# Optimization experiments

Measured on AMD Instinct MI355X. Metric: run time of the kernel, lower is better.

The kernel has to match this reference:

```python
import jax, jax.numpy as jnp
import numpy as np

N_USER, N_ITEM, D = 100000, 50000, 64
H, S, B, L, SUPP, E, HID = 4, 500, 1024, 50, 10000, 1500000, 64

def setup_inputs() -> dict:
    key = jax.random.key(0)
    ks = jax.random.split(key, 24)
    f = lambda k, shp: (jax.random.normal(k, shp, jnp.float32) * 0.1)
    inp = {
        'x': jax.random.randint(ks[0], (B, 2), 0, 50000),
        'history': jax.random.randint(ks[1], (B, L), 0, N_ITEM),
        'history_len': jax.random.randint(ks[2], (B,), 1, L + 1),
        'sample_index': jax.random.randint(ks[3], (H, B, S), 0, SUPP),
        'supp_users': jax.random.randint(ks[4], (SUPP,), 0, N_USER),
        'edge_index': jax.random.randint(ks[5], (2, E), 0, 50000),
        'user_embedding': f(ks[6], (N_USER, D)),
        'item_embedding': f(ks[7], (N_ITEM, D)),
        'wq': f(ks[8], (H, D, D)),
        'wk': f(ks[9], (H, D, D)),
        'wv': f(ks[10], (H, D, D)),
        'w_out_w': f(ks[11], (H * D, D)),
        'gcn_user_w': f(ks[12], (D, D)), 'gcn_user_b': jnp.full((D,), 0.1, jnp.float32),
        'gcn_item_w': f(ks[13], (D, D)), 'gcn_item_b': jnp.full((D,), 0.1, jnp.float32),
        'l1_w': f(ks[14], (4 * D, 2 * HID)), 'l1_b': jnp.full((2 * HID,), 0.1, jnp.float32),
        'l2_w': f(ks[15], (2 * HID, HID)), 'l2_b': jnp.full((HID,), 0.1, jnp.float32),
        'l3_w': f(ks[16], (HID, 1)), 'l3_b': jnp.full((1,), 0.1, jnp.float32),
        'user_bias': jnp.zeros((N_USER, 1), jnp.float32),
        'item_bias': jnp.zeros((N_ITEM, 1), jnp.float32),
    }
    return inp


def _forward(x, history, history_len, sample_index, supp_users, edge_index,
             user_embedding, item_embedding, wq, wk, wv, w_out_w,
             gcn_user_w, gcn_user_b, gcn_item_w, gcn_item_b,
             l1_w, l1_b, l2_w, l2_b, l3_w, l3_b, user_bias, item_bias):
    user_id = x[:, 0]
    item_id = x[:, 1]
    # user init embedding: mean of history item embeddings (original sums unmasked, divides by len)
    user_init_emb = jnp.sum(item_embedding[history], axis=1) / history_len[:, None].astype(jnp.float32)  # [B,D]

    # multi-head RelationGAT over randomly sampled support users
    samp_emb = user_embedding[supp_users[sample_index]]            # [H,B,S,D]
    q = jnp.einsum('bd,hde->hbe', user_init_emb, wq)               # [H,B,D]
    k = jnp.einsum('hbsd,hde->hbse', samp_emb, wk)                 # [H,B,S,D]
    attn = jax.nn.softmax(jnp.einsum('hbe,hbse->hbs', q, k), axis=-1)
    ctx = jnp.einsum('hbs,hbse->hbe', attn, k)                     # [H,B,D]
    gat = jnp.einsum('hbe,hef->hbf', ctx, wv)                      # [H,B,D]
    gat = jnp.transpose(gat, (1, 0, 2)).reshape(gat.shape[1], -1)  # [B,H*D]
    user_emb = gat @ w_out_w                                       # [B,D]

    item_emb = item_embedding[item_id]

    # sparse GCN aggregation via segment_sum (eval mode: no edge dropout)
    eu, ei = edge_index[0], edge_index[1]
    ones_e = jnp.ones((eu.shape[0],), jnp.float32)
    agg_item = jax.ops.segment_sum(item_embedding[ei], eu, num_segments=N_USER)[user_id]
    agg_user = jax.ops.segment_sum(user_embedding[eu], ei, num_segments=N_ITEM)[item_id]
    deg_u = jax.ops.segment_sum(ones_e, eu, num_segments=N_USER)[user_id][:, None] + 1.0
    deg_i = jax.ops.segment_sum(ones_e, ei, num_segments=N_ITEM)[item_id][:, None] + 1.0
    gcn_item_h = agg_item / deg_u
    gcn_user_h = agg_user / deg_i
    gcn_user_out = jax.nn.relu(gcn_user_h @ gcn_user_w + gcn_user_b)
    gcn_item_out = jax.nn.relu(gcn_item_h @ gcn_item_w + gcn_item_b)

    feats = jnp.concatenate([user_emb * item_emb,
                             user_emb * gcn_item_out,
                             gcn_user_out * item_emb,
                             gcn_user_out * gcn_item_out], axis=-1)  # [B,4D]
    h1 = jnp.tanh(feats @ l1_w + l1_b)
    h2 = jnp.tanh(h1 @ l2_w + l2_b)
    score = (h2 @ l3_w + l3_b).reshape(-1)
    return score + user_bias[user_id].reshape(-1) + item_bias[item_id].reshape(-1)


def reference(x, history, history_len, sample_index, supp_users, edge_index,
              user_embedding, item_embedding, wq, wk, wv, w_out_w,
              gcn_user_w, gcn_user_b, gcn_item_w, gcn_item_b,
              l1_w, l1_b, l2_w, l2_b, l3_w, l3_b, user_bias, item_bias):
    return _forward(x, history, history_len, sample_index, supp_users, edge_index,
                    user_embedding, item_embedding, wq, wk, wv, w_out_w,
                    gcn_user_w, gcn_user_b, gcn_item_w, gcn_item_b,
                    l1_w, l1_b, l2_w, l2_b, l3_w, l3_b, user_bias, item_bias)
```

## Files before the change

### kernel.cpp

```cpp
#include <hip/hip_runtime.h>
#include <hip/hip_bf16.h>
#include <math.h>

#define N_USER 100000
#define N_ITEM 50000
#define D 64
#define H 4
#define S 500
#define B 1024
#define L 50
#define SUPP 10000
#define E_EDGES 1500000
#define HID 64
#define N_ID 50000
#define CAP 256

typedef _Float16 half2v __attribute__((ext_vector_type(2)));

#define SUPP_BLKS 625
#define UINIT_BLKS 256
#define PREP1_BLKS 32
#define PREP2_BLKS 64
#define REP_BLKS 4
#define B_UINIT (SUPP_BLKS)
#define B_PREP1 (B_UINIT + UINIT_BLKS)
#define B_PREP2 (B_PREP1 + PREP1_BLKS)
#define B_REP   (B_PREP2 + PREP2_BLKS)
#define SETUP_BLKS (B_REP + REP_BLKS)

__device__ __forceinline__ ushort f2h(float f) {
  _Float16 h = (_Float16)f;
  return __builtin_bit_cast(ushort, h);
}

__global__ void k_setup(const int* x, const int* history, const int* history_len,
                        const int* supp_users, const float* user_embedding,
                        const float* item_embedding, const float* wq, const float* wk,
                        const float* wv, const float* w_out_w,
                        ushort* supp_h, float* uinit, float* Mmat, float* Pmat,
                        int* user_rep, int* item_rep, int* uctr, int* ictr) {
  __shared__ float smem[64 * 65];
  int blk = blockIdx.x, tid = threadIdx.x;
  if (blk < B_UINIT) {
    int i = blk * 256 + tid;
    if (i < SUPP * 16) {
      int r = i >> 4, c = i & 15;
      float4 v = *(const float4*)&user_embedding[(long)supp_users[r] * 64 + c * 4];
      ushort4 o = {f2h(v.x), f2h(v.y), f2h(v.z), f2h(v.w)};
      *(ushort4*)&supp_h[r * 64 + c * 4] = o;
    }
  } else if (blk < B_PREP1) {
    int b = (blk - B_UINIT) * 4 + (tid >> 6);
    int lane = tid & 63, g = lane >> 4, sub = lane & 15;
    float4 acc = {0.f, 0.f, 0.f, 0.f};
    for (int l = g; l < L; l += 4) {
      int idx = history[b * L + l];
      float4 r = *(const float4*)&item_embedding[(long)idx * 64 + sub * 4];
      acc.x += r.x; acc.y += r.y; acc.z += r.z; acc.w += r.w;
    }
    acc.x += __shfl_xor(acc.x, 16); acc.y += __shfl_xor(acc.y, 16);
    acc.z += __shfl_xor(acc.z, 16); acc.w += __shfl_xor(acc.w, 16);
    acc.x += __shfl_xor(acc.x, 32); acc.y += __shfl_xor(acc.y, 32);
    acc.z += __shfl_xor(acc.z, 32); acc.w += __shfl_xor(acc.w, 32);
    if (lane < 16) {
      float inv = 1.f / (float)history_len[b];
      float4 o = {acc.x * inv, acc.y * inv, acc.z * inv, acc.w * inv};
      *(float4*)&uinit[b * 64 + lane * 4] = o;
    }
  } else if (blk < B_PREP2) {
    int local = blk - B_PREP1;
    int h = local >> 3, bx = local & 7;
    for (int i = tid; i < 64 * 64; i += 256) {
      int row = i >> 6, e = i & 63;
      smem[row * 65 + e] = wk[((long)h * 64 + row) * 64 + e];
    }
    __syncthreads();
    for (int k = 0; k < 2; k++) {
      int oidx = bx * 512 + k * 256 + tid;
      int dp = oidx >> 6, d = oidx & 63;
      float acc = 0.f;
      const float* wqrow = wq + ((long)h * 64 + dp) * 64;
#pragma unroll
      for (int e = 0; e < 64; e++) acc += wqrow[e] * smem[d * 65 + e];
      Mmat[((long)h * 64 + dp) * 64 + d] = acc;
    }
  } else if (blk < B_REP) {
    int local = blk - B_PREP2;
    int p = tid >> 6, lane = tid & 63;
    int gp = local * 4 + p;
    int h = gp >> 6, row = gp & 63;
    float* T = smem + p * 64;
    float tf = 0.f;
#pragma unroll
    for (int e = 0; e < 64; e++)
      tf += wk[((long)h * 64 + row) * 64 + e] * wv[((long)h * 64 + e) * 64 + lane];
    T[lane] = tf;
    __syncthreads();
    float acc = 0.f;
#pragma unroll
    for (int f = 0; f < 64; f++)
      acc += T[f] * w_out_w[((long)h * 64 + f) * 64 + lane];
    Pmat[((long)h * 64 + row) * 64 + lane] = acc;
  } else {
    int gi = (blk - B_REP) * 256 + tid;
    if (gi < B) {
      user_rep[x[2 * gi]] = gi;
      item_rep[x[2 * gi + 1]] = gi;
      uctr[gi] = 0;
      ictr[gi] = 0;
    }
  }
}

template <int CTRL>
__device__ __forceinline__ float dpp_add(float v) {
  int t = __builtin_amdgcn_update_dpp(0, __float_as_int(v), CTRL, 0xF, 0xF, true);
  return v + __int_as_float(t);
}
#define DPP_XOR1  0xB1
#define DPP_XOR2  0x4E
#define DPP_HMIR  0x141

__device__ __forceinline__ float dot8h(uint4 rv, half2v k0, half2v k1, half2v k2, half2v k3) {
#if __has_builtin(__builtin_amdgcn_fdot2)
  float d = __builtin_amdgcn_fdot2(__builtin_bit_cast(half2v, rv.x), k0, 0.f, false);
  d = __builtin_amdgcn_fdot2(__builtin_bit_cast(half2v, rv.y), k1, d, false);
  d = __builtin_amdgcn_fdot2(__builtin_bit_cast(half2v, rv.z), k2, d, false);
  d = __builtin_amdgcn_fdot2(__builtin_bit_cast(half2v, rv.w), k3, d, false);
  return d;
#else
  half2v a = __builtin_bit_cast(half2v, rv.x), b = __builtin_bit_cast(half2v, rv.y);
  half2v c = __builtin_bit_cast(half2v, rv.z), e = __builtin_bit_cast(half2v, rv.w);
  return (float)a[0] * (float)k0[0] + (float)a[1] * (float)k0[1] +
         (float)b[0] * (float)k1[0] + (float)b[1] * (float)k1[1] +
         (float)c[0] * (float)k2[0] + (float)c[1] * (float)k2[1] +
         (float)e[0] * (float)k3[0] + (float)e[1] * (float)k3[1];
#endif
}

__device__ __forceinline__ void edge_probe(int u, int it, const int* x,
                                           const int* user_rep, const int* item_rep,
                                           int* uctr, int* ubin, int* ictr, int* ibin) {
  int ru = user_rep[u];
  if ((unsigned)ru < B && x[2 * ru] == u) {
    int pos = atomicAdd(&uctr[ru], 1);
    if (pos < CAP) ubin[ru * CAP + pos] = it;
  }
  int ri = item_rep[it];
  if ((unsigned)ri < B && x[2 * ri + 1] == it) {
    int pos = atomicAdd(&ictr[ri], 1);
    if (pos < CAP) ibin[ri * CAP + pos] = u;
  }
}

__global__ void k_edge(const int* eu, const int* ei, const int* x,
                       const int* user_rep, const int* item_rep,
                       int* uctr, int* ubin, int* ictr, int* ibin) {
  int i = blockIdx.x * 256 + threadIdx.x;
  if (i >= E_EDGES / 2) return;
  int2 u2 = ((const int2*)eu)[i];
  int2 v2 = ((const int2*)ei)[i];
  edge_probe(u2.x, v2.x, x, user_rep, item_rep, uctr, ubin, ictr, ibin);
  edge_probe(u2.y, v2.y, x, user_rep, item_rep, uctr, ubin, ictr, ibin);
}

__global__ void k_attn(const float* uinit, const ushort* supp_h, const int* sample_index,
                       const float* Mmat, const float* Pmat, float* uem4) {
  int tid = threadIdx.x;
  int id = blockIdx.x;
  int h = id >> 10, b = id & 1023;
  int w = tid >> 6, lane = tid & 63;
  int g8 = lane >> 3, sub8 = lane & 7;
  __shared__ float sm_u[64], sm_kq[64], sm_p[256], sm_part[256], sm_den[4];
  __shared__ int sm_sidx[512];

  const int* sidx = sample_index + ((long)h * B + b) * S;
  for (int i = tid; i < 512; i += 256) sm_sidx[i] = (i < S) ? sidx[i] : 0;
  if (tid < 64) sm_u[tid] = uinit[b * 64 + tid];
  __syncthreads();

  const float* Mh = Mmat + h * 64 * 64;
  {
    float p = 0.f;
#pragma unroll
    for (int j = 0; j < 16; j++) p += sm_u[w * 16 + j] * Mh[(w * 16 + j) * 64 + lane];
    sm_p[tid] = p;
  }
  __syncthreads();
  if (tid < 64) sm_kq[tid] = sm_p[tid] + sm_p[64 + tid] + sm_p[128 + tid] + sm_p[192 + tid];
  __syncthreads();

  float4 kqa = *(float4*)&sm_kq[sub8 * 8];
  float4 kqb = *(float4*)&sm_kq[sub8 * 8 + 4];
  half2v k0 = {(_Float16)kqa.x, (_Float16)kqa.y};
  half2v k1 = {(_Float16)kqa.z, (_Float16)kqa.w};
  half2v k2 = {(_Float16)kqb.x, (_Float16)kqb.y};
  half2v k3 = {(_Float16)kqb.z, (_Float16)kqb.w};

  float acc[8] = {0.f, 0.f, 0.f, 0.f, 0.f, 0.f, 0.f, 0.f};
  float den = 0.f;
#pragma unroll 4
  for (int it = 0; it < 16; it++) {
    int s = it * 32 + w * 8 + g8;
    int idx = sm_sidx[s];
    uint4 rv = *(const uint4*)&supp_h[idx * 64 + sub8 * 8];
    float dot = dot8h(rv, k0, k1, k2, k3);
    dot = dpp_add<DPP_XOR1>(dot);
    dot = dpp_add<DPP_XOR2>(dot);
    dot = dpp_add<DPP_HMIR>(dot);
    float e = (s < S) ? __expf(dot) : 0.f;
    den += e;
    half2v r0 = __builtin_bit_cast(half2v, rv.x);
    half2v r1 = __builtin_bit_cast(half2v, rv.y);
    half2v r2 = __builtin_bit_cast(half2v, rv.z);
    half2v r3 = __builtin_bit_cast(half2v, rv.w);
    acc[0] += e * (float)r0[0]; acc[1] += e * (float)r0[1];
    acc[2] += e * (float)r1[0]; acc[3] += e * (float)r1[1];
    acc[4] += e * (float)r2[0]; acc[5] += e * (float)r2[1];
    acc[6] += e * (float)r3[0]; acc[7] += e * (float)r3[1];
  }
#pragma unroll
  for (int j = 0; j < 8; j++) {
    acc[j] += __shfl_xor(acc[j], 8);
    acc[j] += __shfl_xor(acc[j], 16);
    acc[j] += __shfl_xor(acc[j], 32);
  }
  den += __shfl_xor(den, 8); den += __shfl_xor(den, 16); den += __shfl_xor(den, 32);
  if (lane < 8) {
    float4 lo = {acc[0], acc[1], acc[2], acc[3]};
    float4 hi = {acc[4], acc[5], acc[6], acc[7]};
    *(float4*)&sm_part[w * 64 + lane * 8] = lo;
    *(float4*)&sm_part[w * 64 + lane * 8 + 4] = hi;
    if (lane == 0) sm_den[w] = den;
  }
  __syncthreads();
  if (tid < 64) {
    float ws_ = sm_part[tid] + sm_part[64 + tid] + sm_part[128 + tid] + sm_part[192 + tid];
    float dn = sm_den[0] + sm_den[1] + sm_den[2] + sm_den[3];
    sm_u[tid] = ws_ / dn;
  }
  __syncthreads();
  const float* Ph = Pmat + h * 64 * 64;
  {
    float p = 0.f;
#pragma unroll
    for (int j = 0; j < 16; j++) p += sm_u[w * 16 + j] * Ph[(w * 16 + j) * 64 + lane];
    sm_p[tid] = p;
  }
  __syncthreads();
  if (tid < 64)
    uem4[((long)h * B + b) * 64 + tid] =
        sm_p[tid] + sm_p[64 + tid] + sm_p[128 + tid] + sm_p[192 + tid];
}

__global__ void k_final(const int* x, const float* uem4,
                        const float* user_embedding, const float* item_embedding,
                        const int* user_rep, const int* item_rep,
                        const int* uctr, const int* ubin, const int* ictr, const int* ibin,
                        const float* gcn_user_w, const float* gcn_user_b,
                        const float* gcn_item_w, const float* gcn_item_b,
                        const float* l1_w, const float* l1_b,
                        const float* l2_w, const float* l2_b,
                        const float* l3_w, const float* l3_b,
                        const float* user_bias, const float* item_bias, float* out) {
  int b = blockIdx.x, tid = threadIdx.x;
  int side = tid >> 6, lane = tid & 63;
  __shared__ float ue[D], ie[D], agg[2][D], degs[2], guo[D], gio[D],
      feats[4 * D], h1[2 * HID], h2[HID];
  int uid = x[2 * b], iid = x[2 * b + 1];

  {
    int rep = side == 0 ? user_rep[uid] : item_rep[iid];
    int cnt = min((side == 0 ? uctr : ictr)[rep], CAP);
    const int* bin = ((side == 0 ? ubin : ibin)) + rep * CAP;
    const float* emb = side == 0 ? item_embedding : user_embedding;
    float s0 = 0.f, s1 = 0.f, s2 = 0.f, s3 = 0.f;
    int m = 0;
    for (; m + 3 < cnt; m += 4) {
      s0 += emb[(long)bin[m] * 64 + lane];
      s1 += emb[(long)bin[m + 1] * 64 + lane];
      s2 += emb[(long)bin[m + 2] * 64 + lane];
      s3 += emb[(long)bin[m + 3] * 64 + lane];
    }
    for (; m < cnt; m++) s0 += emb[(long)bin[m] * 64 + lane];
    agg[side][lane] = (s0 + s1) + (s2 + s3);
    if (lane == 0) degs[side] = (float)cnt;
  }
  if (tid < D) {
    ue[tid] = uem4[(0L * B + b) * D + tid] + uem4[(1L * B + b) * D + tid] +
              uem4[(2L * B + b) * D + tid] + uem4[(3L * B + b) * D + tid];
    ie[tid] = item_embedding[(long)iid * D + tid];
  }
  __syncthreads();
  if (tid < D) {
    float gih = agg[0][tid] / (degs[0] + 1.f);
    float guh = agg[1][tid] / (degs[1] + 1.f);
    agg[0][tid] = gih;
    agg[1][tid] = guh;
  }
  __syncthreads();
  if (tid < D) {
    float a = 0.f, c = 0.f;
    for (int d = 0; d < D; d++) {
      a += agg[1][d] * gcn_user_w[d * D + tid];
      c += agg[0][d] * gcn_item_w[d * D + tid];
    }
    guo[tid] = fmaxf(a + gcn_user_b[tid], 0.f);
    gio[tid] = fmaxf(c + gcn_item_b[tid], 0.f);
  }
  __syncthreads();
  if (tid < D) {
    feats[tid]         = ue[tid] * ie[tid];
    feats[D + tid]     = ue[tid] * gio[tid];
    feats[2 * D + tid] = guo[tid] * ie[tid];
    feats[3 * D + tid] = guo[tid] * gio[tid];
  }
  __syncthreads();
  {
    float a = 0.f;
    for (int i = 0; i < 4 * D; i++) a += feats[i] * l1_w[i * (2 * HID) + tid];
    h1[tid] = tanhf(a + l1_b[tid]);
  }
  __syncthreads();
  if (tid < HID) {
    float a = 0.f;
    for (int i = 0; i < 2 * HID; i++) a += h1[i] * l2_w[i * HID + tid];
    h2[tid] = tanhf(a + l2_b[tid]);
  }
  __syncthreads();
  if (tid < 64) {
    float v = h2[tid] * l3_w[tid];
#pragma unroll
    for (int off = 32; off > 0; off >>= 1) v += __shfl_xor(v, off);
    if (tid == 0)
      out[b] = v + l3_b[0] + user_bias[uid] + item_bias[iid];
  }
}

extern "C" void kernel_launch(void* const* d_in, const int* in_sizes, int n_in,
                              void* d_out, int out_size, void* d_ws, size_t ws_size,
                              hipStream_t stream) {
  const int* x             = (const int*)d_in[0];
  const int* history       = (const int*)d_in[1];
  const int* history_len   = (const int*)d_in[2];
  const int* sample_index  = (const int*)d_in[3];
  const int* supp_users    = (const int*)d_in[4];
  const int* edge_index    = (const int*)d_in[5];
  const float* user_embedding = (const float*)d_in[6];
  const float* item_embedding = (const float*)d_in[7];
  const float* wq       = (const float*)d_in[8];
  const float* wk       = (const float*)d_in[9];
  const float* wv       = (const float*)d_in[10];
  const float* w_out_w  = (const float*)d_in[11];
  const float* gcn_user_w = (const float*)d_in[12];
  const float* gcn_user_b = (const float*)d_in[13];
  const float* gcn_item_w = (const float*)d_in[14];
  const float* gcn_item_b = (const float*)d_in[15];
  const float* l1_w = (const float*)d_in[16];
  const float* l1_b = (const float*)d_in[17];
  const float* l2_w = (const float*)d_in[18];
  const float* l2_b = (const float*)d_in[19];
  const float* l3_w = (const float*)d_in[20];
  const float* l3_b = (const float*)d_in[21];
  const float* user_bias = (const float*)d_in[22];
  const float* item_bias = (const float*)d_in[23];
  float* out = (float*)d_out;

  float* fws        = (float*)d_ws;
  float* uinit      = fws;
  ushort* supp_h    = (ushort*)(uinit + B * D);
  float* uem4       = uinit + B * D + SUPP * D / 2;
  float* Mmat       = uem4 + (long)H * B * D;
  float* Pmat       = Mmat + H * D * D;
  int* user_rep     = (int*)(Pmat + H * D * D);
  int* item_rep     = user_rep + N_ID;
  int* uctr         = item_rep + N_ID;
  int* ictr         = uctr + B;
  int* ubin         = ictr + B;
  int* ibin         = ubin + B * CAP;

  const int* eu = edge_index;
  const int* ei = edge_index + E_EDGES;

  k_setup<<<SETUP_BLKS, 256, 0, stream>>>(x, history, history_len, supp_users,
                                          user_embedding, item_embedding, wq, wk, wv,
                                          w_out_w, supp_h, uinit, Mmat, Pmat,
                                          user_rep, item_rep, uctr, ictr);
  k_edge<<<(E_EDGES / 2 + 255) / 256, 256, 0, stream>>>(eu, ei, x, user_rep, item_rep,
                                                        uctr, ubin, ictr, ibin);
  k_attn<<<B * H, 256, 0, stream>>>(uinit, supp_h, sample_index, Mmat, Pmat, uem4);
  k_final<<<B, 128, 0, stream>>>(x, uem4, user_embedding, item_embedding,
                                 user_rep, item_rep, uctr, ubin, ictr, ibin,
                                 gcn_user_w, gcn_user_b, gcn_item_w, gcn_item_b,
                                 l1_w, l1_b, l2_w, l2_b, l3_w, l3_b,
                                 user_bias, item_bias, out);
}
```

Baseline: 78.48 us.

## Split attention over two sample halves and move output projection into final kernel

The attention kernel now runs two blocks per (head, batch) pair, each covering half of the 500 samples. Each block writes an unnormalised weighted sum and a softmax denominator. The final kernel merges the halves, normalises, and applies the per-head output projection that used to run inside the attention kernel. The gather loop is hand-pipelined with eight prefetched row indices and loads issued ahead of use, and the edge kernel goes back to one edge per thread. This doubles block count and memory-level parallelism but adds an intermediate buffer round trip and more projection work in the final kernel.

```diff
diff --git a/kernel.cpp b/kernel.cpp
--- a/kernel.cpp
+++ b/kernel.cpp
@@ -14,6 +14,8 @@
 #define HID 64
 #define N_ID 50000
 #define CAP 256
+#define SPLIT 2
+#define SHALF (S / SPLIT)
 
 typedef _Float16 half2v __attribute__((ext_vector_type(2)));
 
@@ -138,9 +140,12 @@
 #endif
 }
 
-__device__ __forceinline__ void edge_probe(int u, int it, const int* x,
-                                           const int* user_rep, const int* item_rep,
-                                           int* uctr, int* ubin, int* ictr, int* ibin) {
+__global__ void k_edge(const int* eu, const int* ei, const int* x,
+                       const int* user_rep, const int* item_rep,
+                       int* uctr, int* ubin, int* ictr, int* ibin) {
+  int i = blockIdx.x * 256 + threadIdx.x;
+  if (i >= E_EDGES) return;
+  int u = eu[i], it = ei[i];
   int ru = user_rep[u];
   if ((unsigned)ru < B && x[2 * ru] == u) {
     int pos = atomicAdd(&uctr[ru], 1);
@@ -153,29 +158,20 @@
   }
 }
 
-__global__ void k_edge(const int* eu, const int* ei, const int* x,
-                       const int* user_rep, const int* item_rep,
-                       int* uctr, int* ubin, int* ictr, int* ibin) {
-  int i = blockIdx.x * 256 + threadIdx.x;
-  if (i >= E_EDGES / 2) return;
-  int2 u2 = ((const int2*)eu)[i];
-  int2 v2 = ((const int2*)ei)[i];
-  edge_probe(u2.x, v2.x, x, user_rep, item_rep, uctr, ubin, ictr, ibin);
-  edge_probe(u2.y, v2.y, x, user_rep, item_rep, uctr, ubin, ictr, ibin);
-}
-
 __global__ void k_attn(const float* uinit, const ushort* supp_h, const int* sample_index,
-                       const float* Mmat, const float* Pmat, float* uem4) {
+                       const float* Mmat, float* uem8, float* den8) {
   int tid = threadIdx.x;
   int id = blockIdx.x;
-  int h = id >> 10, b = id & 1023;
+  int half = id >> 12;
+  int rem = id & 4095;
+  int h = rem >> 10, b = rem & 1023;
   int w = tid >> 6, lane = tid & 63;
   int g8 = lane >> 3, sub8 = lane & 7;
   __shared__ float sm_u[64], sm_kq[64], sm_p[256], sm_part[256], sm_den[4];
-  __shared__ int sm_sidx[512];
-
-  const int* sidx = sample_index + ((long)h * B + b) * S;
-  for (int i = tid; i < 512; i += 256) sm_sidx[i] = (i < S) ? sidx[i] : 0;
+  __shared__ int sm_sidx[256];
+
+  const int* sidx = sample_index + ((long)h * B + b) * S + half * SHALF;
+  sm_sidx[tid] = (tid < SHALF) ? sidx[tid] : 0;
   if (tid < 64) sm_u[tid] = uinit[b * 64 + tid];
   __syncthreads();
 
@@ -197,38 +193,60 @@
   half2v k2 = {(_Float16)kqb.x, (_Float16)kqb.y};
   half2v k3 = {(_Float16)kqb.z, (_Float16)kqb.w};
 
-  float acc[8] = {0.f, 0.f, 0.f, 0.f, 0.f, 0.f, 0.f, 0.f};
+  int sbase = w * 8 + g8;
+  int id0 = sm_sidx[sbase], id1 = sm_sidx[sbase + 32], id2 = sm_sidx[sbase + 64],
+      id3 = sm_sidx[sbase + 96], id4 = sm_sidx[sbase + 128], id5 = sm_sidx[sbase + 160],
+      id6 = sm_sidx[sbase + 192], id7 = sm_sidx[sbase + 224];
+
+  float acc0 = 0.f, acc1 = 0.f, acc2 = 0.f, acc3 = 0.f,
+        acc4 = 0.f, acc5 = 0.f, acc6 = 0.f, acc7 = 0.f;
   float den = 0.f;
-#pragma unroll 4
-  for (int it = 0; it < 16; it++) {
-    int s = it * 32 + w * 8 + g8;
-    int idx = sm_sidx[s];
-    uint4 rv = *(const uint4*)&supp_h[idx * 64 + sub8 * 8];
-    float dot = dot8h(rv, k0, k1, k2, k3);
-    dot = dpp_add<DPP_XOR1>(dot);
-    dot = dpp_add<DPP_XOR2>(dot);
-    dot = dpp_add<DPP_HMIR>(dot);
-    float e = (s < S) ? __expf(dot) : 0.f;
-    den += e;
-    half2v r0 = __builtin_bit_cast(half2v, rv.x);
-    half2v r1 = __builtin_bit_cast(half2v, rv.y);
-    half2v r2 = __builtin_bit_cast(half2v, rv.z);
-    half2v r3 = __builtin_bit_cast(half2v, rv.w);
-    acc[0] += e * (float)r0[0]; acc[1] += e * (float)r0[1];
-    acc[2] += e * (float)r1[0]; acc[3] += e * (float)r1[1];
-    acc[4] += e * (float)r2[0]; acc[5] += e * (float)r2[1];
-    acc[6] += e * (float)r3[0]; acc[7] += e * (float)r3[1];
-  }
-#pragma unroll
-  for (int j = 0; j < 8; j++) {
-    acc[j] += __shfl_xor(acc[j], 8);
-    acc[j] += __shfl_xor(acc[j], 16);
-    acc[j] += __shfl_xor(acc[j], 32);
-  }
+
+#define ROW(IDX) (*(const uint4*)&supp_h[(long)(IDX) * 64 + sub8 * 8])
+#define PROC(V, VALID) { \
+    float dot = dot8h(V, k0, k1, k2, k3); \
+    dot = dpp_add<DPP_XOR1>(dot); \
+    dot = dpp_add<DPP_XOR2>(dot); \
+    dot = dpp_add<DPP_HMIR>(dot); \
+    float e = (VALID) ? __expf(dot) : 0.f;   \
+    den += e; \
+    half2v r0 = __builtin_bit_cast(half2v, (V).x); \
+    half2v r1 = __builtin_bit_cast(half2v, (V).y); \
+    half2v r2 = __builtin_bit_cast(half2v, (V).z); \
+    half2v r3 = __builtin_bit_cast(half2v, (V).w); \
+    acc0 += e * (float)r0[0]; acc1 += e * (float)r0[1]; \
+    acc2 += e * (float)r1[0]; acc3 += e * (float)r1[1]; \
+    acc4 += e * (float)r2[0]; acc5 += e * (float)r2[1]; \
+    acc6 += e * (float)r3[0]; acc7 += e * (float)r3[1]; \
+  }
+
+  uint4 va = ROW(id0);
+  uint4 vb = ROW(id1);
+  uint4 vc = ROW(id2);
+  uint4 vd = ROW(id3);
+  PROC(va, true); va = ROW(id4);
+  PROC(vb, true); vb = ROW(id5);
+  PROC(vc, true); vc = ROW(id6);
+  PROC(vd, true); vd = ROW(id7);
+  PROC(va, true);
+  PROC(vb, true);
+  PROC(vc, true);
+  PROC(vd, sbase + 224 < SHALF);
+#undef PROC
+#undef ROW
+
+  acc0 += __shfl_xor(acc0, 8); acc0 += __shfl_xor(acc0, 16); acc0 += __shfl_xor(acc0, 32);
+  acc1 += __shfl_xor(acc1, 8); acc1 += __shfl_xor(acc1, 16); acc1 += __shfl_xor(acc1, 32);
+  acc2 += __shfl_xor(acc2, 8); acc2 += __shfl_xor(acc2, 16); acc2 += __shfl_xor(acc2, 32);
+  acc3 += __shfl_xor(acc3, 8); acc3 += __shfl_xor(acc3, 16); acc3 += __shfl_xor(acc3, 32);
+  acc4 += __shfl_xor(acc4, 8); acc4 += __shfl_xor(acc4, 16); acc4 += __shfl_xor(acc4, 32);
+  acc5 += __shfl_xor(acc5, 8); acc5 += __shfl_xor(acc5, 16); acc5 += __shfl_xor(acc5, 32);
+  acc6 += __shfl_xor(acc6, 8); acc6 += __shfl_xor(acc6, 16); acc6 += __shfl_xor(acc6, 32);
+  acc7 += __shfl_xor(acc7, 8); acc7 += __shfl_xor(acc7, 16); acc7 += __shfl_xor(acc7, 32);
   den += __shfl_xor(den, 8); den += __shfl_xor(den, 16); den += __shfl_xor(den, 32);
   if (lane < 8) {
-    float4 lo = {acc[0], acc[1], acc[2], acc[3]};
-    float4 hi = {acc[4], acc[5], acc[6], acc[7]};
+    float4 lo = {acc0, acc1, acc2, acc3};
+    float4 hi = {acc4, acc5, acc6, acc7};
     *(float4*)&sm_part[w * 64 + lane * 8] = lo;
     *(float4*)&sm_part[w * 64 + lane * 8 + 4] = hi;
     if (lane == 0) sm_den[w] = den;
@@ -236,24 +254,14 @@
   __syncthreads();
   if (tid < 64) {
     float ws_ = sm_part[tid] + sm_part[64 + tid] + sm_part[128 + tid] + sm_part[192 + tid];
-    float dn = sm_den[0] + sm_den[1] + sm_den[2] + sm_den[3];
-    sm_u[tid] = ws_ / dn;
-  }
-  __syncthreads();
-  const float* Ph = Pmat + h * 64 * 64;
-  {
-    float p = 0.f;
-#pragma unroll
-    for (int j = 0; j < 16; j++) p += sm_u[w * 16 + j] * Ph[(w * 16 + j) * 64 + lane];
-    sm_p[tid] = p;
-  }
-  __syncthreads();
-  if (tid < 64)
-    uem4[((long)h * B + b) * 64 + tid] =
-        sm_p[tid] + sm_p[64 + tid] + sm_p[128 + tid] + sm_p[192 + tid];
-}
-
-__global__ void k_final(const int* x, const float* uem4,
+    uem8[((long)(half * H + h) * B + b) * 64 + tid] = ws_;
+    if (tid == 0)
+      den8[(half * H + h) * B + b] = sm_den[0] + sm_den[1] + sm_den[2] + sm_den[3];
+  }
+}
+
+__global__ void k_final(const int* x, const float* uem8, const float* den8,
+                        const float* Pmat,
                         const float* user_embedding, const float* item_embedding,
                         const int* user_rep, const int* item_rep,
                         const int* uctr, const int* ubin, const int* ictr, const int* ibin,
@@ -266,8 +274,16 @@
   int b = blockIdx.x, tid = threadIdx.x;
   int side = tid >> 6, lane = tid & 63;
   __shared__ float ue[D], ie[D], agg[2][D], degs[2], guo[D], gio[D],
-      feats[4 * D], h1[2 * HID], h2[HID];
+      feats[4 * D], h1[2 * HID], h2[HID], wsum[4][D], pue[128];
   int uid = x[2 * b], iid = x[2 * b + 1];
+
+  for (int k = tid; k < 4 * D; k += 128) {
+    int hh = k >> 6, d = k & 63;
+    float a = uem8[((long)(0 * H + hh) * B + b) * 64 + d] +
+              uem8[((long)(1 * H + hh) * B + b) * 64 + d];
+    float dn = den8[(0 * H + hh) * B + b] + den8[(1 * H + hh) * B + b];
+    wsum[hh][d] = a / dn;
+  }
 
   {
     int rep = side == 0 ? user_rep[uid] : item_rep[iid];
@@ -286,13 +302,23 @@
     agg[side][lane] = (s0 + s1) + (s2 + s3);
     if (lane == 0) degs[side] = (float)cnt;
   }
+  if (tid < D) ie[tid] = item_embedding[(long)iid * D + tid];
+  __syncthreads();
+
+  {
+    int hh0 = side * 2, e = lane;
+    float p = 0.f;
+#pragma unroll
+    for (int hh = 0; hh < 2; hh++) {
+      const float* Ph = Pmat + (long)(hh0 + hh) * 64 * 64;
+#pragma unroll
+      for (int d = 0; d < 64; d++) p += wsum[hh0 + hh][d] * Ph[d * 64 + e];
+    }
+    pue[tid] = p;
+  }
+  __syncthreads();
   if (tid < D) {
-    ue[tid] = uem4[(0L * B + b) * D + tid] + uem4[(1L * B + b) * D + tid] +
-              uem4[(2L * B + b) * D + tid] + uem4[(3L * B + b) * D + tid];
-    ie[tid] = item_embedding[(long)iid * D + tid];
-  }
-  __syncthreads();
-  if (tid < D) {
+    ue[tid] = pue[tid] + pue[64 + tid];
     float gih = agg[0][tid] / (degs[0] + 1.f);
     float guh = agg[1][tid] / (degs[1] + 1.f);
     agg[0][tid] = gih;
@@ -369,8 +395,9 @@
   float* fws        = (float*)d_ws;
   float* uinit      = fws;
   ushort* supp_h    = (ushort*)(uinit + B * D);
-  float* uem4       = uinit + B * D + SUPP * D / 2;
-  float* Mmat       = uem4 + (long)H * B * D;
+  float* uem8       = uinit + B * D + SUPP * D / 2;
+  float* den8       = uem8 + (long)SPLIT * H * B * D;
+  float* Mmat       = den8 + SPLIT * H * B;
   float* Pmat       = Mmat + H * D * D;
   int* user_rep     = (int*)(Pmat + H * D * D);
   int* item_rep     = user_rep + N_ID;
@@ -386,10 +413,10 @@
                                           user_embedding, item_embedding, wq, wk, wv,
                                           w_out_w, supp_h, uinit, Mmat, Pmat,
                                           user_rep, item_rep, uctr, ictr);
-  k_edge<<<(E_EDGES / 2 + 255) / 256, 256, 0, stream>>>(eu, ei, x, user_rep, item_rep,
-                                                        uctr, ubin, ictr, ibin);
-  k_attn<<<B * H, 256, 0, stream>>>(uinit, supp_h, sample_index, Mmat, Pmat, uem4);
-  k_final<<<B, 128, 0, stream>>>(x, uem4, user_embedding, item_embedding,
+  k_edge<<<(E_EDGES + 255) / 256, 256, 0, stream>>>(eu, ei, x, user_rep, item_rep,
+                                                    uctr, ubin, ictr, ibin);
+  k_attn<<<SPLIT * B * H, 256, 0, stream>>>(uinit, supp_h, sample_index, Mmat, uem8, den8);
+  k_final<<<B, 128, 0, stream>>>(x, uem8, den8, Pmat, user_embedding, item_embedding,
                                  user_rep, item_rep, uctr, ubin, ictr, ibin,
                                  gcn_user_w, gcn_user_b, gcn_item_w, gcn_item_b,
                                  l1_w, l1_b, l2_w, l2_b, l3_w, l3_b,
```

Measured after the change: 81.89 us. 4.3% more time.
